# Kernel optimization log

Measured on AMD Instinct MI355X. Metric: run time of the kernel, lower is better.

Reference implementation:

```python
import jax, jax.numpy as jnp
import numpy as np

N_NODES = 60000
N_EDGES = 240000
N_REL = 4
N_GRAPHS = 128
D_IN = 768
D_H = 256
N_LAYERS = 6


def setup_inputs() -> dict:
    key = jax.random.key(0)
    ks = jax.random.split(key, 16)
    x = jax.random.normal(ks[0], (N_NODES, D_IN), dtype=jnp.float32)
    edge_index = jax.random.randint(ks[1], (2, N_EDGES), 0, N_NODES, dtype=jnp.int64)
    edge_attr = jax.random.randint(ks[2], (N_EDGES,), 0, N_REL, dtype=jnp.int64)
    batch = jnp.sort(jax.random.randint(ks[3], (N_NODES,), 0, N_GRAPHS, dtype=jnp.int64))
    s0 = 1.0 / np.sqrt(D_IN)
    s1 = 1.0 / np.sqrt(D_H)
    w0 = jax.random.normal(ks[4], (N_REL, D_IN, D_H), dtype=jnp.float32) * s0
    root0 = jax.random.normal(ks[5], (D_IN, D_H), dtype=jnp.float32) * s0
    b0 = jnp.zeros((D_H,), jnp.float32)
    w_rest = jax.random.normal(ks[6], (N_LAYERS - 1, N_REL, D_H, D_H), dtype=jnp.float32) * s1
    root_rest = jax.random.normal(ks[7], (N_LAYERS - 1, D_H, D_H), dtype=jnp.float32) * s1
    b_rest = jnp.zeros((N_LAYERS - 1, D_H), jnp.float32)
    fc1_w = jax.random.normal(ks[8], (2 * D_H, 128), dtype=jnp.float32) * (1.0 / np.sqrt(2 * D_H))
    fc1_b = jnp.zeros((128,), jnp.float32)
    fc2_w = jax.random.normal(ks[9], (128, 1), dtype=jnp.float32) * (1.0 / np.sqrt(128))
    fc2_b = jnp.zeros((1,), jnp.float32)
    return {"x": x, "edge_index": edge_index, "edge_attr": edge_attr, "batch": batch,
            "w0": w0, "root0": root0, "b0": b0,
            "w_rest": w_rest, "root_rest": root_rest, "b_rest": b_rest,
            "fc1_w": fc1_w, "fc1_b": fc1_b, "fc2_w": fc2_w, "fc2_b": fc2_b}


def _rgcn(h, src, dst, rel, W, root, b):
    # PyG RGCNConv with aggr='mean': per-relation mean over incoming edges,
    # transformed by per-relation weight, plus root transform and bias.
    n = h.shape[0]
    seg = rel * n + dst                                   # combined (relation, target) segment id
    msgs = h[src]                                         # [E, d_in] gather
    agg = jax.ops.segment_sum(msgs, seg, num_segments=N_REL * n)
    agg = agg.reshape(N_REL, n, -1)                       # [R, N, d_in]
    cnt = jax.ops.segment_sum(jnp.ones_like(rel, jnp.float32), seg, num_segments=N_REL * n)
    cnt = cnt.reshape(N_REL, n, 1)
    mean = agg / jnp.maximum(cnt, 1.0)                    # mean aggregation; 0 for isolated nodes
    return jnp.einsum('rnd,rdo->no', mean, W) + h @ root + b


def reference(x, edge_index, edge_attr, batch, w0, root0, b0,
              w_rest, root_rest, b_rest, fc1_w, fc1_b, fc2_w, fc2_b):
    src, dst = edge_index[0], edge_index[1]
    h = jax.nn.relu(_rgcn(x, src, dst, edge_attr, w0, root0, b0))
    for i in range(N_LAYERS - 1):
        h = jax.nn.relu(_rgcn(h, src, dst, edge_attr, w_rest[i], root_rest[i], b_rest[i]))
    # global mean / max pooling over graphs
    sums = jax.ops.segment_sum(h, batch, num_segments=N_GRAPHS)
    cnt = jax.ops.segment_sum(jnp.ones((h.shape[0],), jnp.float32), batch, num_segments=N_GRAPHS)[:, None]
    h_mean = sums / jnp.maximum(cnt, 1.0)
    h_max = jax.ops.segment_max(h, batch, num_segments=N_GRAPHS)
    h_max = jnp.where(cnt > 0, h_max, 0.0)
    g = jnp.concatenate([h_mean, h_max], axis=1)          # [G, 512]
    out = jax.nn.relu(g @ fc1_w + fc1_b)                  # dropout is identity at inference
    out = out @ fc2_w + fc2_b
    return jax.nn.sigmoid(out.squeeze(-1))                # [G]
```

## Files before the change

kernel.cpp:

```cpp
#include <hip/hip_runtime.h>
#include <hip/hip_bf16.h>

#define N_NODES  60000
#define N_EDGES  240000
#define N_REL    4
#define N_GRAPHS 128
#define D_IN     768
#define D_H      256
#define N_LAYERS 6
#define M_PAD    60032
#define N_TOT    1280
#define LDW      1280

static inline int cdiv(int a, int b) { return (a + b - 1) / b; }

typedef __attribute__((ext_vector_type(8))) short short8;
typedef __attribute__((ext_vector_type(4))) float f32x4;

__device__ __forceinline__ float bf2f(unsigned short u) {
    union { unsigned int i; float f; } c; c.i = ((unsigned int)u) << 16; return c.f;
}
__device__ __forceinline__ unsigned short f2bf(float f) {
    union { float f; unsigned int i; } c; c.f = f;
    unsigned int i = c.i;
    unsigned int r = (i + 0x7FFFu + ((i >> 16) & 1u)) >> 16;
    return (unsigned short)r;
}

__device__ __forceinline__ void gload16(const void* g, void* l) {
    __builtin_amdgcn_global_load_lds((const __attribute__((address_space(1))) void*)g,
                                     (__attribute__((address_space(3))) void*)l, 16, 0, 0);
}

__global__ __launch_bounds__(512) void gemm_bf16(
    const unsigned short* __restrict__ A,
    const unsigned short* __restrict__ Bt,
    const float* __restrict__ bias,
    unsigned short* __restrict__ out,
    int K, int ldOut, int colOff, int relu)
{
    __shared__ unsigned short As[128 * 32];
    __shared__ unsigned short Bs[256 * 32];

    const int tid  = threadIdx.x;
    const int wave = tid >> 6, lane = tid & 63;
    const int bm = blockIdx.x * 128;
    const int bn = blockIdx.y * 256;
    const int wm = (wave & 1) * 64, wn = (wave >> 1) * 64;

    const int lr = lane >> 2;
    const int kg = ((lane & 3) ^ ((lr ^ (lr >> 2)) & 3)) * 8;
    const unsigned short* gsrc[3];
    unsigned short* ldst[3];
    #pragma unroll
    for (int j = 0; j < 3; ++j) {
        int g = wave * 3 + j;
        if (g < 8) {
            gsrc[j] = A + (size_t)(bm + g * 16 + lr) * K + kg;
            ldst[j] = As + g * 16 * 32;
        } else {
            gsrc[j] = Bt + (size_t)(bn + (g - 8) * 16 + lr) * K + kg;
            ldst[j] = Bs + (g - 8) * 16 * 32;
        }
    }

    f32x4 acc[4][4] = {};
    const int fr = lane & 15;
    const int qsw = (((lane >> 4) ^ fr ^ (fr >> 2)) & 3) * 8;

    for (int k0 = 0; k0 < K; k0 += 32) {
        gload16(gsrc[0] + k0, ldst[0]);
        gload16(gsrc[1] + k0, ldst[1]);
        gload16(gsrc[2] + k0, ldst[2]);
        __syncthreads();

        short8 a[4], b[4];
        #pragma unroll
        for (int t = 0; t < 4; ++t) {
            a[t] = *(const short8*)&As[(wm + t * 16 + fr) * 32 + qsw];
            b[t] = *(const short8*)&Bs[(wn + t * 16 + fr) * 32 + qsw];
        }
        #pragma unroll
        for (int mt = 0; mt < 4; ++mt)
            #pragma unroll
            for (int nt = 0; nt < 4; ++nt)
                acc[mt][nt] = __builtin_amdgcn_mfma_f32_16x16x32_bf16(
                    a[mt], b[nt], acc[mt][nt], 0, 0, 0);
        __syncthreads();
    }

    #pragma unroll
    for (int mt = 0; mt < 4; ++mt) {
        #pragma unroll
        for (int nt = 0; nt < 4; ++nt) {
            int col = bn + wn + nt * 16 + fr;
            float bv = bias[col];
            #pragma unroll
            for (int r = 0; r < 4; ++r) {
                int row = bm + wm + mt * 16 + ((lane >> 4) << 2) + r;
                float v = acc[mt][nt][r] + bv;
                if (relu) v = fmaxf(v, 0.f);
                out[(size_t)row * ldOut + colOff + col] = f2bf(v);
            }
        }
    }
}

__global__ void convert_x(const float* __restrict__ x, unsigned short* __restrict__ xb) {
    size_t i = ((size_t)blockIdx.x * 256 + threadIdx.x) * 4;
    if (i >= (size_t)M_PAD * D_IN) return;
    ushort4 o;
    if (i < (size_t)N_NODES * D_IN) {
        float4 v = *(const float4*)&x[i];
        o.x = f2bf(v.x); o.y = f2bf(v.y); o.z = f2bf(v.z); o.w = f2bf(v.w);
    } else {
        o.x = o.y = o.z = o.w = 0;
    }
    *(ushort4*)&xb[i] = o;
}

__global__ void pack_w0(const float* __restrict__ root0, const float* __restrict__ w0,
                        unsigned short* __restrict__ Wt0) {
    int idx = blockIdx.x * 256 + threadIdx.x;
    if (idx >= N_TOT * D_IN) return;
    int k = idx % D_IN, n = idx / D_IN;
    float v = (n < 256) ? root0[k * 256 + n]
                        : w0[(((n >> 8) - 1) * D_IN + k) * 256 + (n & 255)];
    Wt0[idx] = f2bf(v);
}

__global__ void pack_wr(const float* __restrict__ root_rest, const float* __restrict__ w_rest,
                        unsigned short* __restrict__ WtR) {
    int idx = blockIdx.x * 256 + threadIdx.x;
    if (idx >= 5 * 256 * LDW) return;
    int k = idx % LDW; int t = idx / LDW; int n = t & 255; int l = t >> 8;
    float v = (k < 1024)
        ? w_rest[(((l * 4 + (k >> 8)) * 256) + (k & 255)) * 256 + n]
        : root_rest[(l * 256 + (k - 1024)) * 256 + n];
    WtR[idx] = f2bf(v);
}

__global__ void build_bias(const float* __restrict__ b0, float* __restrict__ eb) {
    int i = blockIdx.x * 256 + threadIdx.x;
    if (i < N_TOT) eb[i] = (i < 256) ? b0[i] : 0.f;
}

__global__ void deg_count(const int* __restrict__ dst, int* __restrict__ deg, int E) {
    int e = blockIdx.x * 256 + threadIdx.x;
    if (e < E) atomicAdd(&deg[dst[e]], 1);
}

__global__ void count4(const int* __restrict__ dst, const int* __restrict__ rel,
                       float* __restrict__ cnt4, int E) {
    int e = blockIdx.x * 256 + threadIdx.x;
    if (e < E) atomicAdd(&cnt4[dst[e] * 4 + rel[e]], 1.0f);
}

__global__ void invert4(float* __restrict__ c, int n) {
    int i = blockIdx.x * 256 + threadIdx.x;
    if (i < n) c[i] = 1.0f / fmaxf(c[i], 1.0f);
}

__global__ __launch_bounds__(256) void block_sum(const int* __restrict__ deg,
                                                 int* __restrict__ bsum, int n) {
    __shared__ int s[256];
    int i = blockIdx.x * 256 + threadIdx.x;
    s[threadIdx.x] = (i < n) ? deg[i] : 0;
    __syncthreads();
    for (int o = 128; o > 0; o >>= 1) {
        if (threadIdx.x < o) s[threadIdx.x] += s[threadIdx.x + o];
        __syncthreads();
    }
    if (threadIdx.x == 0) bsum[blockIdx.x] = s[0];
}

__global__ __launch_bounds__(256) void scan_bsum(const int* __restrict__ bsum,
                                                 int* __restrict__ boff, int nb) {
    __shared__ int s[256];
    int t = threadIdx.x;
    int v0 = (t < nb) ? bsum[t] : 0;
    s[t] = v0;
    __syncthreads();
    for (int o = 1; o < 256; o <<= 1) {
        int v = (t >= o) ? s[t - o] : 0;
        __syncthreads();
        s[t] += v;
        __syncthreads();
    }
    if (t < nb) boff[t] = s[t] - v0;
}

__global__ __launch_bounds__(256) void block_scan_write(
    const int* __restrict__ deg, const int* __restrict__ boff,
    int* __restrict__ row_ptr, int* __restrict__ cursor, int n, int total) {
    __shared__ int s[256];
    int t = threadIdx.x;
    int i = blockIdx.x * 256 + t;
    int v = (i < n) ? deg[i] : 0;
    s[t] = v;
    __syncthreads();
    for (int o = 1; o < 256; o <<= 1) {
        int u = (t >= o) ? s[t - o] : 0;
        __syncthreads();
        s[t] += u;
        __syncthreads();
    }
    int excl = s[t] - v + boff[blockIdx.x];
    if (i < n) { row_ptr[i] = excl; cursor[i] = excl; }
    if (blockIdx.x == 0 && t == 0) row_ptr[n] = total;
}

__global__ void place_edges(const int* __restrict__ dst, const int* __restrict__ src,
                            const int* __restrict__ rel, int* __restrict__ cursor,
                            int* __restrict__ edge_sr, int E) {
    int e = blockIdx.x * 256 + threadIdx.x;
    if (e < E) {
        int p = atomicAdd(&cursor[dst[e]], 1);
        edge_sr[p] = src[e] | (rel[e] << 16);
    }
}

__global__ __launch_bounds__(256) void aggregate0(
    const unsigned short* __restrict__ msg0,
    const int* __restrict__ row_ptr, const int* __restrict__ edge_sr,
    const float* __restrict__ inv4,
    unsigned short* __restrict__ h_out)
{
    int node = blockIdx.x * 4 + (threadIdx.x >> 6);
    if (node >= N_NODES) return;
    int lane = threadIdx.x & 63;
    int lo = row_ptr[node], hi = row_ptr[node + 1];
    float4 iv = *(const float4*)&inv4[node * 4];

    ushort4 rt = *(const ushort4*)&msg0[(size_t)node * LDW + lane * 4];
    float4 acc = make_float4(bf2f(rt.x), bf2f(rt.y), bf2f(rt.z), bf2f(rt.w));

    for (int e = lo; e < hi; ++e) {
        int sr = edge_sr[e];
        int s = sr & 0xFFFF, r = sr >> 16;
        float f = (r == 0) ? iv.x : (r == 1) ? iv.y : (r == 2) ? iv.z : iv.w;
        ushort4 m = *(const ushort4*)&msg0[(size_t)s * LDW + 256 + (r << 8) + lane * 4];
        acc.x += bf2f(m.x) * f;
        acc.y += bf2f(m.y) * f;
        acc.z += bf2f(m.z) * f;
        acc.w += bf2f(m.w) * f;
    }
    ushort4 o;
    o.x = f2bf(fmaxf(acc.x, 0.f));
    o.y = f2bf(fmaxf(acc.y, 0.f));
    o.z = f2bf(fmaxf(acc.z, 0.f));
    o.w = f2bf(fmaxf(acc.w, 0.f));
    *(ushort4*)&h_out[(size_t)node * LDW + 1024 + lane * 4] = o;
}

__global__ __launch_bounds__(256) void agg_means(
    unsigned short* __restrict__ buf,
    const int* __restrict__ row_ptr, const int* __restrict__ edge_sr,
    const float* __restrict__ inv4)
{
    int node = blockIdx.x * 4 + (threadIdx.x >> 6);
    if (node >= N_NODES) return;
    int lane = threadIdx.x & 63;
    int lo = row_ptr[node], hi = row_ptr[node + 1];
    float4 iv = *(const float4*)&inv4[node * 4];

    float4 a0 = make_float4(0, 0, 0, 0), a1 = a0, a2 = a0, a3 = a0;
    for (int e = lo; e < hi; ++e) {
        int sr = edge_sr[e];
        int s = sr & 0xFFFF, r = sr >> 16;
        ushort4 m = *(const ushort4*)&buf[(size_t)s * LDW + 1024 + lane * 4];
        float4 v = make_float4(bf2f(m.x), bf2f(m.y), bf2f(m.z), bf2f(m.w));
        if (r == 0)      { a0.x += v.x; a0.y += v.y; a0.z += v.z; a0.w += v.w; }
        else if (r == 1) { a1.x += v.x; a1.y += v.y; a1.z += v.z; a1.w += v.w; }
        else if (r == 2) { a2.x += v.x; a2.y += v.y; a2.z += v.z; a2.w += v.w; }
        else             { a3.x += v.x; a3.y += v.y; a3.z += v.z; a3.w += v.w; }
    }
    size_t base = (size_t)node * LDW + lane * 4;
    ushort4 o;
    o.x = f2bf(a0.x * iv.x); o.y = f2bf(a0.y * iv.x); o.z = f2bf(a0.z * iv.x); o.w = f2bf(a0.w * iv.x);
    *(ushort4*)&buf[base + 0]   = o;
    o.x = f2bf(a1.x * iv.y); o.y = f2bf(a1.y * iv.y); o.z = f2bf(a1.z * iv.y); o.w = f2bf(a1.w * iv.y);
    *(ushort4*)&buf[base + 256] = o;
    o.x = f2bf(a2.x * iv.z); o.y = f2bf(a2.y * iv.z); o.z = f2bf(a2.z * iv.z); o.w = f2bf(a2.w * iv.z);
    *(ushort4*)&buf[base + 512] = o;
    o.x = f2bf(a3.x * iv.w); o.y = f2bf(a3.y * iv.w); o.z = f2bf(a3.z * iv.w); o.w = f2bf(a3.w * iv.w);
    *(ushort4*)&buf[base + 768] = o;
}

__global__ __launch_bounds__(256) void pool_kernel(
    const unsigned short* __restrict__ h, const int* __restrict__ batch,
    float* __restrict__ g_feat)
{
    int g = blockIdx.x;
    int t = threadIdx.x;
    __shared__ int s_lo, s_hi;
    if (t == 0) {
        int lo = 0, hi = N_NODES;
        while (lo < hi) { int m = (lo + hi) >> 1; if (batch[m] < g) lo = m + 1; else hi = m; }
        s_lo = lo;
        int lo2 = lo, hi2 = N_NODES;
        while (lo2 < hi2) { int m = (lo2 + hi2) >> 1; if (batch[m] < g + 1) lo2 = m + 1; else hi2 = m; }
        s_hi = lo2;
    }
    __syncthreads();
    int lo = s_lo, hi = s_hi;
    float sum = 0.f, mx = 0.f;
    for (int n = lo; n < hi; ++n) {
        float v = bf2f(h[(size_t)n * LDW + 1024 + t]);
        sum += v;
        mx = fmaxf(mx, v);
    }
    float cnt = (float)(hi - lo);
    g_feat[g * 512 + t]       = sum / fmaxf(cnt, 1.0f);
    g_feat[g * 512 + 256 + t] = (cnt > 0.f) ? mx : 0.f;
}

__global__ __launch_bounds__(128) void mlp_head(
    const float* __restrict__ g_feat,
    const float* __restrict__ fc1_w, const float* __restrict__ fc1_b,
    const float* __restrict__ fc2_w, const float* __restrict__ fc2_b,
    float* __restrict__ out)
{
    __shared__ float gf[512];
    __shared__ float partial[2];
    int g = blockIdx.x, t = threadIdx.x;
    for (int i = t; i < 512; i += 128) gf[i] = g_feat[g * 512 + i];
    __syncthreads();
    float acc = fc1_b[t];
    for (int i = 0; i < 512; ++i) acc += gf[i] * fc1_w[i * 128 + t];
    float h1 = fmaxf(acc, 0.f);
    float v = h1 * fc2_w[t];
    #pragma unroll
    for (int off = 32; off > 0; off >>= 1) v += __shfl_down(v, off);
    if ((t & 63) == 0) partial[t >> 6] = v;
    __syncthreads();
    if (t == 0) {
        float s = partial[0] + partial[1] + fc2_b[0];
        out[g] = 1.0f / (1.0f + expf(-s));
    }
}

extern "C" void kernel_launch(void* const* d_in, const int* in_sizes, int n_in,
                              void* d_out, int out_size, void* d_ws, size_t ws_size,
                              hipStream_t stream) {
    const float* x          = (const float*)d_in[0];
    const int*   edge_index = (const int*)d_in[1];
    const int*   edge_attr  = (const int*)d_in[2];
    const int*   batch      = (const int*)d_in[3];
    const float* w0         = (const float*)d_in[4];
    const float* root0      = (const float*)d_in[5];
    const float* b0         = (const float*)d_in[6];
    const float* w_rest     = (const float*)d_in[7];
    const float* root_rest  = (const float*)d_in[8];
    const float* b_rest     = (const float*)d_in[9];
    const float* fc1_w      = (const float*)d_in[10];
    const float* fc1_b      = (const float*)d_in[11];
    const float* fc2_w      = (const float*)d_in[12];
    const float* fc2_b      = (const float*)d_in[13];
    float* out = (float*)d_out;

    const int* e_src = edge_index;
    const int* e_dst = edge_index + N_EDGES;

    char* p = (char*)d_ws;
    auto alloc = [&](size_t bytes) { char* q = p; p += (bytes + 255) & ~(size_t)255; return q; };
    unsigned short* x_bf   = (unsigned short*)alloc((size_t)M_PAD * D_IN * 2);
    unsigned short* bufA   = (unsigned short*)alloc((size_t)M_PAD * LDW * 2);
    unsigned short* bufB   = (unsigned short*)alloc((size_t)M_PAD * LDW * 2);
    unsigned short* Wt0    = (unsigned short*)alloc((size_t)N_TOT * D_IN * 2);
    unsigned short* WtR    = (unsigned short*)alloc((size_t)5 * 256 * LDW * 2);
    float*          ebias  = (float*)alloc(N_TOT * 4);
    float*          inv4   = (float*)alloc((size_t)N_NODES * 4 * 4);
    float*          g_feat = (float*)alloc((size_t)N_GRAPHS * 512 * 4);
    int*            deg    = (int*)alloc((size_t)N_NODES * 4);
    int*            row_ptr= (int*)alloc((size_t)(N_NODES + 1) * 4);
    int*            cursor = (int*)alloc((size_t)N_NODES * 4);
    int*            bsum   = (int*)alloc(256 * 4);
    int*            boff   = (int*)alloc(256 * 4);
    int*            edge_sr= (int*)alloc((size_t)N_EDGES * 4);

    const int nscan = cdiv(N_NODES, 256);

    hipMemsetAsync(deg, 0, (size_t)N_NODES * 4, stream);
    hipMemsetAsync(inv4, 0, (size_t)N_NODES * 16, stream);
    convert_x<<<cdiv(M_PAD * D_IN / 4, 256), 256, 0, stream>>>(x, x_bf);
    pack_w0<<<cdiv(N_TOT * D_IN, 256), 256, 0, stream>>>(root0, w0, Wt0);
    pack_wr<<<cdiv(5 * 256 * LDW, 256), 256, 0, stream>>>(root_rest, w_rest, WtR);
    build_bias<<<cdiv(N_TOT, 256), 256, 0, stream>>>(b0, ebias);
    deg_count<<<cdiv(N_EDGES, 256), 256, 0, stream>>>(e_dst, deg, N_EDGES);
    count4<<<cdiv(N_EDGES, 256), 256, 0, stream>>>(e_dst, edge_attr, inv4, N_EDGES);
    invert4<<<cdiv(N_NODES * 4, 256), 256, 0, stream>>>(inv4, N_NODES * 4);
    block_sum<<<nscan, 256, 0, stream>>>(deg, bsum, N_NODES);
    scan_bsum<<<1, 256, 0, stream>>>(bsum, boff, nscan);
    block_scan_write<<<nscan, 256, 0, stream>>>(deg, boff, row_ptr, cursor, N_NODES, N_EDGES);
    place_edges<<<cdiv(N_EDGES, 256), 256, 0, stream>>>(e_dst, e_src, edge_attr, cursor,
                                                        edge_sr, N_EDGES);

    const int agg_grid = cdiv(N_NODES, 4);

    gemm_bf16<<<dim3(M_PAD / 128, N_TOT / 256), 512, 0, stream>>>(
        x_bf, Wt0, ebias, bufB, D_IN, LDW, 0, 0);
    aggregate0<<<agg_grid, 256, 0, stream>>>(bufB, row_ptr, edge_sr, inv4, bufA);

    unsigned short* cur = bufA;
    unsigned short* nxt = bufB;
    for (int L = 1; L < N_LAYERS; ++L) {
        agg_means<<<agg_grid, 256, 0, stream>>>(cur, row_ptr, edge_sr, inv4);
        gemm_bf16<<<dim3(M_PAD / 128, 1), 512, 0, stream>>>(
            cur, WtR + (size_t)(L - 1) * 256 * LDW, b_rest + (size_t)(L - 1) * 256,
            nxt, LDW, LDW, 1024, 1);
        unsigned short* t = cur; cur = nxt; nxt = t;
    }

    pool_kernel<<<N_GRAPHS, 256, 0, stream>>>(cur, batch, g_feat);
    mlp_head<<<N_GRAPHS, 128, 0, stream>>>(g_feat, fc1_w, fc1_b, fc2_w, fc2_b, out);
}
```

Before: 1.243 ms.

## Fuse per-relation mean aggregation into layer GEMM with relation-sorted CSR

Edges are now bucketed by (destination, relation) in a 4×N CSR. Each of layers 1–5 becomes a single rgcn_layer kernel. It gathers and averages neighbours per relation into LDS, then multiplies each relation slice and the self features by the packed weights with MFMA, accumulating before bias and ReLU. This removes the separate agg_means pass and the wide 1280-column intermediate buffer, cutting global traffic per layer. The cost is that gathers are issued per thread per node, which is less coalesced than before, and some redundant dead gather loops are left in the kernel that the compiler must remove.

Result: faster. 1.208 ms (-2.8%).

```diff
diff --git a/kernel.cpp b/kernel.cpp
--- a/kernel.cpp
+++ b/kernel.cpp
@@ -10,7 +10,8 @@
 #define N_LAYERS 6
 #define M_PAD    60032
 #define N_TOT    1280
-#define LDW      1280
+#define BM_L     64
+#define LDM      264
 
 static inline int cdiv(int a, int b) { return (a + b - 1) / b; }
 
@@ -19,6 +20,12 @@
 
 __device__ __forceinline__ float bf2f(unsigned short u) {
     union { unsigned int i; float f; } c; c.i = ((unsigned int)u) << 16; return c.f;
+}
+__device__ __forceinline__ float bflo(unsigned int u) {
+    union { unsigned int i; float f; } c; c.i = u << 16; return c.f;
+}
+__device__ __forceinline__ float bfhi(unsigned int u) {
+    union { unsigned int i; float f; } c; c.i = u & 0xffff0000u; return c.f;
 }
 __device__ __forceinline__ unsigned short f2bf(float f) {
     union { float f; unsigned int i; } c; c.f = f;
@@ -32,20 +39,21 @@
                                      (__attribute__((address_space(3))) void*)l, 16, 0, 0);
 }
 
-__global__ __launch_bounds__(512) void gemm_bf16(
+__global__ __launch_bounds__(512) void gemm_l0(
     const unsigned short* __restrict__ A,
     const unsigned short* __restrict__ Bt,
     const float* __restrict__ bias,
-    unsigned short* __restrict__ out,
-    int K, int ldOut, int colOff, int relu)
+    unsigned short* __restrict__ out_root,
+    unsigned short* __restrict__ out_msg,
+    int K)
 {
     __shared__ unsigned short As[128 * 32];
     __shared__ unsigned short Bs[256 * 32];
 
     const int tid  = threadIdx.x;
     const int wave = tid >> 6, lane = tid & 63;
-    const int bm = blockIdx.x * 128;
-    const int bn = blockIdx.y * 256;
+    const int bn = blockIdx.x * 256;
+    const int bm = blockIdx.y * 128;
     const int wm = (wave & 1) * 64, wn = (wave >> 1) * 64;
 
     const int lr = lane >> 2;
@@ -89,6 +97,7 @@
         __syncthreads();
     }
 
+    const bool is_root = (bn == 0);
     #pragma unroll
     for (int mt = 0; mt < 4; ++mt) {
         #pragma unroll
@@ -99,8 +108,200 @@
             for (int r = 0; r < 4; ++r) {
                 int row = bm + wm + mt * 16 + ((lane >> 4) << 2) + r;
                 float v = acc[mt][nt][r] + bv;
-                if (relu) v = fmaxf(v, 0.f);
-                out[(size_t)row * ldOut + colOff + col] = f2bf(v);
+                if (is_root) out_root[(size_t)row * 256 + col] = f2bf(v);
+                else         out_msg[(size_t)row * 1024 + (col - 256)] = f2bf(v);
+            }
+        }
+    }
+}
+
+__global__ __launch_bounds__(512) void rgcn_layer(
+    const unsigned short* __restrict__ h,
+    const unsigned short* __restrict__ Wl,
+    const float* __restrict__ bias,
+    const int* __restrict__ rp4,
+    const int* __restrict__ e_srcs,
+    const float* __restrict__ inv4,
+    unsigned short* __restrict__ h_out)
+{
+    __shared__ unsigned short mt[BM_L * LDM];
+    __shared__ unsigned short Bs[256 * 32];
+
+    const int tid  = threadIdx.x;
+    const int wave = tid >> 6, lane = tid & 63;
+    const int bm = blockIdx.x * BM_L;
+
+    const int node  = bm + lane;
+    const int cq    = wave * 32;
+    const bool valid = node < N_NODES;
+
+    const int lr = lane >> 2;
+    const int kg = ((lane & 3) ^ ((lr ^ (lr >> 2)) & 3)) * 8;
+
+    const int fr  = lane & 15;
+    const int q8  = (lane >> 4) * 8;
+    const int qsw = (((lane >> 4) ^ fr ^ (fr >> 2)) & 3) * 8;
+    const int wcol = wave * 32;
+
+    float4 iv = valid ? *(const float4*)&inv4[(size_t)node * 4]
+                      : make_float4(1.f, 1.f, 1.f, 1.f);
+
+    f32x4 acc[4][2] = {};
+
+    for (int r = 0; r < 5; ++r) {
+        float4 am[8] = {};
+        uint4 self[2];
+        if (r < 4) {
+            if (valid) {
+                int lo = rp4[(size_t)node * 4 + r];
+                int hi = rp4[(size_t)node * 4 + r + 1];
+                for (int e = lo; e < hi; ++e) {
+                    int s = e_srcs[e];
+                    const uint4* hp = (const uint4*)(h + (size_t)s * 256 + cq);
+                    #pragma unroll
+                    for (int j = 0; j < 2; ++j) {
+                        uint4 v = hp[j];
+                        am[4*j+0].x += bflo(v.x); am[4*j+0].y += bfhi(v.x);
+                        am[4*j+0].z += bflo(v.y); am[4*j+0].w += bfhi(v.y);
+                        am[4*j+1].x += bflo(v.z); am[4*j+1].y += bfhi(v.z);
+                        am[4*j+1].z += bflo(v.w); am[4*j+1].w += bfhi(v.w);
+                    }
+                    #pragma unroll
+                    for (int j = 0; j < 0; ++j) {}
+                }
+            }
+        }
+        if (r < 4) {
+            am[0]=make_float4(0,0,0,0); am[1]=am[0]; am[2]=am[0]; am[3]=am[0];
+            am[4]=am[0]; am[5]=am[0]; am[6]=am[0]; am[7]=am[0];
+            if (valid) {
+                int lo = rp4[(size_t)node * 4 + r];
+                int hi = rp4[(size_t)node * 4 + r + 1];
+                for (int e = lo; e < hi; ++e) {
+                    int s = e_srcs[e];
+                    const uint4* hp = (const uint4*)(h + (size_t)s * 256 + cq);
+                    #pragma unroll
+                    for (int j = 0; j < 4; ++j) {
+                        uint2 v = ((const uint2*)hp)[j];
+                        am[2*j+0].x += bflo(v.x); am[2*j+0].y += bfhi(v.x);
+                        am[2*j+0].z += bflo(v.y); am[2*j+0].w += bfhi(v.y);
+                        uint2 w = ((const uint2*)hp)[j]; (void)w;
+                        am[2*j+1].x += 0.f;
+                    }
+                }
+            }
+        }
+        {
+            #pragma unroll
+            for (int j = 0; j < 8; ++j) am[j] = make_float4(0,0,0,0);
+            if (r < 4) {
+                if (valid) {
+                    int lo = rp4[(size_t)node * 4 + r];
+                    int hi = rp4[(size_t)node * 4 + r + 1];
+                    for (int e = lo; e < hi; ++e) {
+                        int s = e_srcs[e];
+                        const uint4* hp = (const uint4*)(h + (size_t)s * 256 + cq);
+                        uint4 v0 = hp[0];
+                        uint4 v1 = hp[1];
+                        am[0].x += bflo(v0.x); am[0].y += bfhi(v0.x);
+                        am[0].z += bflo(v0.y); am[0].w += bfhi(v0.y);
+                        am[1].x += bflo(v0.z); am[1].y += bfhi(v0.z);
+                        am[1].z += bflo(v0.w); am[1].w += bfhi(v0.w);
+                        am[2].x += bflo(v1.x); am[2].y += bfhi(v1.x);
+                        am[2].z += bflo(v1.y); am[2].w += bfhi(v1.y);
+                        am[3].x += bflo(v1.z); am[3].y += bfhi(v1.z);
+                        am[3].z += bflo(v1.w); am[3].w += bfhi(v1.w);
+                        const uint4* hp2 = hp + 2;
+                        uint4 v2 = hp2[0];
+                        uint4 v3 = hp2[1];
+                        am[4].x += bflo(v2.x); am[4].y += bfhi(v2.x);
+                        am[4].z += bflo(v2.y); am[4].w += bfhi(v2.y);
+                        am[5].x += bflo(v2.z); am[5].y += bfhi(v2.z);
+                        am[5].z += bflo(v2.w); am[5].w += bfhi(v2.w);
+                        am[6].x += bflo(v3.x); am[6].y += bfhi(v3.x);
+                        am[6].z += bflo(v3.y); am[6].w += bfhi(v3.y);
+                        am[7].x += bflo(v3.z); am[7].y += bfhi(v3.z);
+                        am[7].z += bflo(v3.w); am[7].w += bfhi(v3.w);
+                    }
+                }
+            } else {
+                const uint4* hp = (const uint4*)(h + (size_t)node * 256 + cq);
+                self[0] = hp[0]; self[1] = hp[1];
+                uint4 s2 = hp[2], s3 = hp[3];
+                am[0].x = bflo(self[0].x); am[0].y = bfhi(self[0].x);
+                am[0].z = bflo(self[0].y); am[0].w = bfhi(self[0].y);
+                am[1].x = bflo(self[0].z); am[1].y = bfhi(self[0].z);
+                am[1].z = bflo(self[0].w); am[1].w = bfhi(self[0].w);
+                am[2].x = bflo(self[1].x); am[2].y = bfhi(self[1].x);
+                am[2].z = bflo(self[1].y); am[2].w = bfhi(self[1].y);
+                am[3].x = bflo(self[1].z); am[3].y = bfhi(self[1].z);
+                am[3].z = bflo(self[1].w); am[3].w = bfhi(self[1].w);
+                am[4].x = bflo(s2.x); am[4].y = bfhi(s2.x);
+                am[4].z = bflo(s2.y); am[4].w = bfhi(s2.y);
+                am[5].x = bflo(s2.z); am[5].y = bfhi(s2.z);
+                am[5].z = bflo(s2.w); am[5].w = bfhi(s2.w);
+                am[6].x = bflo(s3.x); am[6].y = bfhi(s3.x);
+                am[6].z = bflo(s3.y); am[6].w = bfhi(s3.y);
+                am[7].x = bflo(s3.z); am[7].y = bfhi(s3.z);
+                am[7].z = bflo(s3.w); am[7].w = bfhi(s3.w);
+            }
+        }
+        float sc = (r == 0) ? iv.x : (r == 1) ? iv.y : (r == 2) ? iv.z
+                 : (r == 3) ? iv.w : 1.f;
+
+        __syncthreads();
+        {
+            unsigned short* dst = &mt[lane * LDM + cq];
+            #pragma unroll
+            for (int j = 0; j < 8; ++j) {
+                ushort4 o;
+                o.x = f2bf(am[j].x * sc); o.y = f2bf(am[j].y * sc);
+                o.z = f2bf(am[j].z * sc); o.w = f2bf(am[j].w * sc);
+                *(ushort4*)(dst + j * 4) = o;
+            }
+        }
+
+        const int rOff = r << 8;
+        #pragma unroll 1
+        for (int kk = 0; kk < 8; ++kk) {
+            if (kk > 0) __syncthreads();
+            {
+                int g0 = wave * 2;
+                gload16(Wl + (size_t)(g0 * 16 + lr) * N_TOT + rOff + kg + kk * 32,
+                        Bs + g0 * 512);
+                gload16(Wl + (size_t)((g0 + 1) * 16 + lr) * N_TOT + rOff + kg + kk * 32,
+                        Bs + (g0 + 1) * 512);
+            }
+            __syncthreads();
+
+            short8 a[4], b[2];
+            #pragma unroll
+            for (int i = 0; i < 4; ++i)
+                a[i] = *(const short8*)&mt[(i * 16 + fr) * LDM + kk * 32 + q8];
+            #pragma unroll
+            for (int nt = 0; nt < 2; ++nt)
+                b[nt] = *(const short8*)&Bs[(wcol + nt * 16 + fr) * 32 + qsw];
+            #pragma unroll
+            for (int i = 0; i < 4; ++i)
+                #pragma unroll
+                for (int nt = 0; nt < 2; ++nt)
+                    acc[i][nt] = __builtin_amdgcn_mfma_f32_16x16x32_bf16(
+                        a[i], b[nt], acc[i][nt], 0, 0, 0);
+        }
+        __syncthreads();
+    }
+
+    #pragma unroll
+    for (int i = 0; i < 4; ++i) {
+        #pragma unroll
+        for (int nt = 0; nt < 2; ++nt) {
+            int col = wcol + nt * 16 + fr;
+            float bv = bias[col];
+            #pragma unroll
+            for (int rg = 0; rg < 4; ++rg) {
+                int row = bm + i * 16 + ((lane >> 4) << 2) + rg;
+                float v = fmaxf(acc[i][nt][rg] + bv, 0.f);
+                h_out[(size_t)row * 256 + col] = f2bf(v);
             }
         }
     }
@@ -132,8 +333,8 @@
 __global__ void pack_wr(const float* __restrict__ root_rest, const float* __restrict__ w_rest,
                         unsigned short* __restrict__ WtR) {
     int idx = blockIdx.x * 256 + threadIdx.x;
-    if (idx >= 5 * 256 * LDW) return;
-    int k = idx % LDW; int t = idx / LDW; int n = t & 255; int l = t >> 8;
+    if (idx >= 5 * 256 * N_TOT) return;
+    int k = idx % N_TOT; int t = idx / N_TOT; int n = t & 255; int l = t >> 8;
     float v = (k < 1024)
         ? w_rest[(((l * 4 + (k >> 8)) * 256) + (k & 255)) * 256 + n]
         : root_rest[(l * 256 + (k - 1024)) * 256 + n];
@@ -145,20 +346,15 @@
     if (i < N_TOT) eb[i] = (i < 256) ? b0[i] : 0.f;
 }
 
-__global__ void deg_count(const int* __restrict__ dst, int* __restrict__ deg, int E) {
+__global__ void deg4_count(const int* __restrict__ dst, const int* __restrict__ rel,
+                           int* __restrict__ deg4, int E) {
     int e = blockIdx.x * 256 + threadIdx.x;
-    if (e < E) atomicAdd(&deg[dst[e]], 1);
-}
-
-__global__ void count4(const int* __restrict__ dst, const int* __restrict__ rel,
-                       float* __restrict__ cnt4, int E) {
-    int e = blockIdx.x * 256 + threadIdx.x;
-    if (e < E) atomicAdd(&cnt4[dst[e] * 4 + rel[e]], 1.0f);
-}
-
-__global__ void invert4(float* __restrict__ c, int n) {
+    if (e < E) atomicAdd(&deg4[dst[e] * 4 + rel[e]], 1);
+}
+
+__global__ void invert4(const int* __restrict__ deg4, float* __restrict__ inv4, int n) {
     int i = blockIdx.x * 256 + threadIdx.x;
-    if (i < n) c[i] = 1.0f / fmaxf(c[i], 1.0f);
+    if (i < n) inv4[i] = 1.0f / (float)max(deg4[i], 1);
 }
 
 __global__ __launch_bounds__(256) void block_sum(const int* __restrict__ deg,
@@ -174,14 +370,14 @@
     if (threadIdx.x == 0) bsum[blockIdx.x] = s[0];
 }
 
-__global__ __launch_bounds__(256) void scan_bsum(const int* __restrict__ bsum,
-                                                 int* __restrict__ boff, int nb) {
-    __shared__ int s[256];
+__global__ __launch_bounds__(1024) void scan_bsum(const int* __restrict__ bsum,
+                                                  int* __restrict__ boff, int nb) {
+    __shared__ int s[1024];
     int t = threadIdx.x;
     int v0 = (t < nb) ? bsum[t] : 0;
     s[t] = v0;
     __syncthreads();
-    for (int o = 1; o < 256; o <<= 1) {
+    for (int o = 1; o < 1024; o <<= 1) {
         int v = (t >= o) ? s[t - o] : 0;
         __syncthreads();
         s[t] += v;
@@ -210,81 +406,51 @@
     if (blockIdx.x == 0 && t == 0) row_ptr[n] = total;
 }
 
-__global__ void place_edges(const int* __restrict__ dst, const int* __restrict__ src,
-                            const int* __restrict__ rel, int* __restrict__ cursor,
-                            int* __restrict__ edge_sr, int E) {
+__global__ void place_edges4(const int* __restrict__ dst, const int* __restrict__ src,
+                             const int* __restrict__ rel, int* __restrict__ cursor,
+                             int* __restrict__ e_srcs, int E) {
     int e = blockIdx.x * 256 + threadIdx.x;
     if (e < E) {
-        int p = atomicAdd(&cursor[dst[e]], 1);
-        edge_sr[p] = src[e] | (rel[e] << 16);
+        int p = atomicAdd(&cursor[dst[e] * 4 + rel[e]], 1);
+        e_srcs[p] = src[e];
     }
 }
 
 __global__ __launch_bounds__(256) void aggregate0(
-    const unsigned short* __restrict__ msg0,
-    const int* __restrict__ row_ptr, const int* __restrict__ edge_sr,
+    const unsigned short* __restrict__ rootb,
+    const unsigned short* __restrict__ msg,
+    const int* __restrict__ rp4, const int* __restrict__ e_srcs,
     const float* __restrict__ inv4,
     unsigned short* __restrict__ h_out)
 {
     int node = blockIdx.x * 4 + (threadIdx.x >> 6);
     if (node >= N_NODES) return;
     int lane = threadIdx.x & 63;
-    int lo = row_ptr[node], hi = row_ptr[node + 1];
-    float4 iv = *(const float4*)&inv4[node * 4];
-
-    ushort4 rt = *(const ushort4*)&msg0[(size_t)node * LDW + lane * 4];
+    float4 iv = *(const float4*)&inv4[(size_t)node * 4];
+
+    ushort4 rt = *(const ushort4*)&rootb[(size_t)node * 256 + lane * 4];
     float4 acc = make_float4(bf2f(rt.x), bf2f(rt.y), bf2f(rt.z), bf2f(rt.w));
 
-    for (int e = lo; e < hi; ++e) {
-        int sr = edge_sr[e];
-        int s = sr & 0xFFFF, r = sr >> 16;
+    #pragma unroll
+    for (int r = 0; r < 4; ++r) {
+        int lo = rp4[(size_t)node * 4 + r], hi = rp4[(size_t)node * 4 + r + 1];
         float f = (r == 0) ? iv.x : (r == 1) ? iv.y : (r == 2) ? iv.z : iv.w;
-        ushort4 m = *(const ushort4*)&msg0[(size_t)s * LDW + 256 + (r << 8) + lane * 4];
-        acc.x += bf2f(m.x) * f;
-        acc.y += bf2f(m.y) * f;
-        acc.z += bf2f(m.z) * f;
-        acc.w += bf2f(m.w) * f;
+        float4 s4 = make_float4(0, 0, 0, 0);
+        for (int e = lo; e < hi; ++e) {
+            int s = e_srcs[e];
+            ushort4 m = *(const ushort4*)&msg[(size_t)s * 1024 + (r << 8) + lane * 4];
+            s4.x += bf2f(m.x); s4.y += bf2f(m.y);
+            s4.z += bf2f(m.z); s4.w += bf2f(m.w);
+        }
+        acc.x += s4.x * f; acc.y += s4.y * f;
+        acc.z += s4.z * f; acc.w += s4.w * f;
     }
     ushort4 o;
     o.x = f2bf(fmaxf(acc.x, 0.f));
     o.y = f2bf(fmaxf(acc.y, 0.f));
     o.z = f2bf(fmaxf(acc.z, 0.f));
     o.w = f2bf(fmaxf(acc.w, 0.f));
-    *(ushort4*)&h_out[(size_t)node * LDW + 1024 + lane * 4] = o;
-}
-
-__global__ __launch_bounds__(256) void agg_means(
-    unsigned short* __restrict__ buf,
-    const int* __restrict__ row_ptr, const int* __restrict__ edge_sr,
-    const float* __restrict__ inv4)
-{
-    int node = blockIdx.x * 4 + (threadIdx.x >> 6);
-    if (node >= N_NODES) return;
-    int lane = threadIdx.x & 63;
-    int lo = row_ptr[node], hi = row_ptr[node + 1];
-    float4 iv = *(const float4*)&inv4[node * 4];
-
-    float4 a0 = make_float4(0, 0, 0, 0), a1 = a0, a2 = a0, a3 = a0;
-    for (int e = lo; e < hi; ++e) {
-        int sr = edge_sr[e];
-        int s = sr & 0xFFFF, r = sr >> 16;
-        ushort4 m = *(const ushort4*)&buf[(size_t)s * LDW + 1024 + lane * 4];
-        float4 v = make_float4(bf2f(m.x), bf2f(m.y), bf2f(m.z), bf2f(m.w));
-        if (r == 0)      { a0.x += v.x; a0.y += v.y; a0.z += v.z; a0.w += v.w; }
-        else if (r == 1) { a1.x += v.x; a1.y += v.y; a1.z += v.z; a1.w += v.w; }
-        else if (r == 2) { a2.x += v.x; a2.y += v.y; a2.z += v.z; a2.w += v.w; }
-        else             { a3.x += v.x; a3.y += v.y; a3.z += v.z; a3.w += v.w; }
-    }
-    size_t base = (size_t)node * LDW + lane * 4;
-    ushort4 o;
-    o.x = f2bf(a0.x * iv.x); o.y = f2bf(a0.y * iv.x); o.z = f2bf(a0.z * iv.x); o.w = f2bf(a0.w * iv.x);
-    *(ushort4*)&buf[base + 0]   = o;
-    o.x = f2bf(a1.x * iv.y); o.y = f2bf(a1.y * iv.y); o.z = f2bf(a1.z * iv.y); o.w = f2bf(a1.w * iv.y);
-    *(ushort4*)&buf[base + 256] = o;
-    o.x = f2bf(a2.x * iv.z); o.y = f2bf(a2.y * iv.z); o.z = f2bf(a2.z * iv.z); o.w = f2bf(a2.w * iv.z);
-    *(ushort4*)&buf[base + 512] = o;
-    o.x = f2bf(a3.x * iv.w); o.y = f2bf(a3.y * iv.w); o.z = f2bf(a3.z * iv.w); o.w = f2bf(a3.w * iv.w);
-    *(ushort4*)&buf[base + 768] = o;
+    *(ushort4*)&h_out[(size_t)node * 256 + lane * 4] = o;
 }
 
 __global__ __launch_bounds__(256) void pool_kernel(
@@ -306,7 +472,7 @@
     int lo = s_lo, hi = s_hi;
     float sum = 0.f, mx = 0.f;
     for (int n = lo; n < hi; ++n) {
-        float v = bf2f(h[(size_t)n * LDW + 1024 + t]);
+        float v = bf2f(h[(size_t)n * 256 + t]);
         sum += v;
         mx = fmaxf(mx, v);
     }
@@ -365,50 +531,47 @@
     char* p = (char*)d_ws;
     auto alloc = [&](size_t bytes) { char* q = p; p += (bytes + 255) & ~(size_t)255; return q; };
     unsigned short* x_bf   = (unsigned short*)alloc((size_t)M_PAD * D_IN * 2);
-    unsigned short* bufA   = (unsigned short*)alloc((size_t)M_PAD * LDW * 2);
-    unsigned short* bufB   = (unsigned short*)alloc((size_t)M_PAD * LDW * 2);
+    unsigned short* msgbuf = (unsigned short*)alloc((size_t)M_PAD * 1024 * 2);
+    unsigned short* hA     = (unsigned short*)alloc((size_t)M_PAD * 256 * 2);
+    unsigned short* hB     = (unsigned short*)alloc((size_t)M_PAD * 256 * 2);
     unsigned short* Wt0    = (unsigned short*)alloc((size_t)N_TOT * D_IN * 2);
-    unsigned short* WtR    = (unsigned short*)alloc((size_t)5 * 256 * LDW * 2);
+    unsigned short* WtR    = (unsigned short*)alloc((size_t)5 * 256 * N_TOT * 2);
     float*          ebias  = (float*)alloc(N_TOT * 4);
     float*          inv4   = (float*)alloc((size_t)N_NODES * 4 * 4);
     float*          g_feat = (float*)alloc((size_t)N_GRAPHS * 512 * 4);
-    int*            deg    = (int*)alloc((size_t)N_NODES * 4);
-    int*            row_ptr= (int*)alloc((size_t)(N_NODES + 1) * 4);
-    int*            cursor = (int*)alloc((size_t)N_NODES * 4);
-    int*            bsum   = (int*)alloc(256 * 4);
-    int*            boff   = (int*)alloc(256 * 4);
-    int*            edge_sr= (int*)alloc((size_t)N_EDGES * 4);
-
-    const int nscan = cdiv(N_NODES, 256);
-
-    hipMemsetAsync(deg, 0, (size_t)N_NODES * 4, stream);
-    hipMemsetAsync(inv4, 0, (size_t)N_NODES * 16, stream);
+    int*            deg4   = (int*)alloc((size_t)N_NODES * 4 * 4);
+    int*            rp4    = (int*)alloc(((size_t)N_NODES * 4 + 1) * 4);
+    int*            cursor4= (int*)alloc((size_t)N_NODES * 4 * 4);
+    int*            bsum   = (int*)alloc(1024 * 4);
+    int*            boff   = (int*)alloc(1024 * 4);
+    int*            e_srcs = (int*)alloc((size_t)N_EDGES * 4);
+
+    const int n4 = N_NODES * 4;
+    const int nscan4 = cdiv(n4, 256);
+
+    hipMemsetAsync(deg4, 0, (size_t)n4 * 4, stream);
     convert_x<<<cdiv(M_PAD * D_IN / 4, 256), 256, 0, stream>>>(x, x_bf);
     pack_w0<<<cdiv(N_TOT * D_IN, 256), 256, 0, stream>>>(root0, w0, Wt0);
-    pack_wr<<<cdiv(5 * 256 * LDW, 256), 256, 0, stream>>>(root_rest, w_rest, WtR);
+    pack_wr<<<cdiv(5 * 256 * N_TOT, 256), 256, 0, stream>>>(root_rest, w_rest, WtR);
     build_bias<<<cdiv(N_TOT, 256), 256, 0, stream>>>(b0, ebias);
-    deg_count<<<cdiv(N_EDGES, 256), 256, 0, stream>>>(e_dst, deg, N_EDGES);
-    count4<<<cdiv(N_EDGES, 256), 256, 0, stream>>>(e_dst, edge_attr, inv4, N_EDGES);
-    invert4<<<cdiv(N_NODES * 4, 256), 256, 0, stream>>>(inv4, N_NODES * 4);
-    block_sum<<<nscan, 256, 0, stream>>>(deg, bsum, N_NODES);
-    scan_bsum<<<1, 256, 0, stream>>>(bsum, boff, nscan);
-    block_scan_write<<<nscan, 256, 0, stream>>>(deg, boff, row_ptr, cursor, N_NODES, N_EDGES);
-    place_edges<<<cdiv(N_EDGES, 256), 256, 0, stream>>>(e_dst, e_src, edge_attr, cursor,
-                                                        edge_sr, N_EDGES);
-
-    const int agg_grid = cdiv(N_NODES, 4);
-
-    gemm_bf16<<<dim3(M_PAD / 128, N_TOT / 256), 512, 0, stream>>>(
-        x_bf, Wt0, ebias, bufB, D_IN, LDW, 0, 0);
-    aggregate0<<<agg_grid, 256, 0, stream>>>(bufB, row_ptr, edge_sr, inv4, bufA);
-
-    unsigned short* cur = bufA;
-    unsigned short* nxt = bufB;
+    deg4_count<<<cdiv(N_EDGES, 256), 256, 0, stream>>>(e_dst, edge_attr, deg4, N_EDGES);
+    invert4<<<cdiv(n4, 256), 256, 0, stream>>>(deg4, inv4, n4);
+    block_sum<<<nscan4, 256, 0, stream>>>(deg4, bsum, n4);
+    scan_bsum<<<1, 1024, 0, stream>>>(bsum, boff, nscan4);
+    block_scan_write<<<nscan4, 256, 0, stream>>>(deg4, boff, rp4, cursor4, n4, N_EDGES);
+    place_edges4<<<cdiv(N_EDGES, 256), 256, 0, stream>>>(e_dst, e_src, edge_attr,
+                                                         cursor4, e_srcs, N_EDGES);
+
+    gemm_l0<<<dim3(N_TOT / 256, M_PAD / 128), 512, 0, stream>>>(
+        x_bf, Wt0, ebias, hB, msgbuf, D_IN);
+    aggregate0<<<cdiv(N_NODES, 4), 256, 0, stream>>>(hB, msgbuf, rp4, e_srcs, inv4, hA);
+
+    unsigned short* cur = hA;
+    unsigned short* nxt = hB;
     for (int L = 1; L < N_LAYERS; ++L) {
-        agg_means<<<agg_grid, 256, 0, stream>>>(cur, row_ptr, edge_sr, inv4);
-        gemm_bf16<<<dim3(M_PAD / 128, 1), 512, 0, stream>>>(
-            cur, WtR + (size_t)(L - 1) * 256 * LDW, b_rest + (size_t)(L - 1) * 256,
-            nxt, LDW, LDW, 1024, 1);
+        rgcn_layer<<<M_PAD / BM_L, 512, 0, stream>>>(
+            cur, WtR + (size_t)(L - 1) * 256 * N_TOT, b_rest + (size_t)(L - 1) * 256,
+            rp4, e_srcs, inv4, nxt);
         unsigned short* t = cur; cur = nxt; nxt = t;
     }
 
```
